# Kernel optimization log

Measured on AMD Instinct MI355X. Metric: run time of the kernel, lower is better.

The kernel has to match this reference:

```python
import jax, jax.numpy as jnp
import numpy as np
from jax import lax

Z_DIM = 64
ZS_SIZE = [[1, 1]] * 12 + [[2, 1]] + [[2, 2]] * 11 + [[4, 2]] + [[4, 4]] * 11  # 36 embeddings
FILTER = [[16, 16]] * 6 + [[16, 32]] + [[32, 32]] * 5 + [[32, 64]] + [[64, 64]] * 5  # 18 blocks
OFFS = np.cumsum([0] + [h * k for h, k in ZS_SIZE]).tolist()  # 242 z-vectors total


def _hyper(Z, hn_w2, hn_b2, hn_w1, hn_b1):
    # Batched HyperNetwork: Z [n, 64] -> kernels [n, 16, 16, 3, 3]
    n = Z.shape[0]
    h_in = (Z @ hn_w2 + hn_b2).reshape(n, 16, Z_DIM)            # [n, 16, 64]
    h_fin = jnp.einsum('nid,do->nio', h_in, hn_w1) + hn_b1       # [n, 16, 144]
    return h_fin.reshape(n, 16, 16, 3, 3)


def _make_w(z_all, idx, hn_w2, hn_b2, hn_w1, hn_b1):
    # Assemble conv weight [h*16, k*16, 3, 3] from h*k hypernet tiles (cat dim=1 over k, dim=0 over h)
    h, k = ZS_SIZE[idx]
    Z = z_all[OFFS[idx]:OFFS[idx] + h * k]
    K = _hyper(Z, hn_w2, hn_b2, hn_w1, hn_b1)                    # [h*k, 16, 16, 3, 3]
    K = K.reshape(h, k, 16, 16, 3, 3).transpose(0, 2, 1, 3, 4, 5)
    return K.reshape(h * 16, k * 16, 3, 3)


def _conv(x, w, stride, pad):
    return lax.conv_general_dilated(x, w, (stride, stride), [(pad, pad), (pad, pad)],
                                    dimension_numbers=('NCHW', 'OIHW', 'NCHW'))


def _bn(x, i, g, b, m, v):
    # eval-mode BatchNorm2d with running stats; params padded to 64 channels
    C = x.shape[1]
    gg = g[i, :C].reshape(1, C, 1, 1)
    bb = b[i, :C].reshape(1, C, 1, 1)
    mm = m[i, :C].reshape(1, C, 1, 1)
    vv = v[i, :C].reshape(1, C, 1, 1)
    return (x - mm) * (gg * lax.rsqrt(vv + 1e-5)) + bb


def setup_inputs() -> dict:
    key = jax.random.key(0)
    ks = jax.random.split(key, 16)
    B = 1024
    x = jax.random.normal(ks[0], (B, 3, 32, 32), jnp.float32)
    conv1_w = jax.random.normal(ks[1], (16, 3, 3, 3), jnp.float32) / np.float32(np.sqrt(27.0))
    conv1_b = jnp.zeros((16,), jnp.float32)
    n_bn = 37  # bn1 + 2 per block
    bn_gamma = jnp.ones((n_bn, 64), jnp.float32)
    bn_beta = jnp.zeros((n_bn, 64), jnp.float32)
    bn_mean = jnp.zeros((n_bn, 64), jnp.float32)
    bn_var = jnp.ones((n_bn, 64), jnp.float32)
    hn_w2 = jax.random.normal(ks[2], (Z_DIM, 16 * Z_DIM), jnp.float32) * 0.04
    hn_b2 = jax.random.normal(ks[3], (16 * Z_DIM,), jnp.float32) * 0.01
    hn_w1 = jax.random.normal(ks[4], (Z_DIM, 16 * 9), jnp.float32) * 0.04
    hn_b1 = jax.random.normal(ks[5], (16 * 9,), jnp.float32) * 0.01
    z_all = jax.random.normal(ks[6], (OFFS[-1], Z_DIM), jnp.float32)
    res_w6 = jax.random.normal(ks[7], (32, 16, 1, 1), jnp.float32) * 0.25
    res_b6 = jnp.zeros((32,), jnp.float32)
    res_w12 = jax.random.normal(ks[8], (64, 32, 1, 1), jnp.float32) * 0.18
    res_b12 = jnp.zeros((64,), jnp.float32)
    fin_w = jax.random.normal(ks[9], (10, 64), jnp.float32) * 0.1
    fin_b = jnp.zeros((10,), jnp.float32)
    return {"x": x, "conv1_w": conv1_w, "conv1_b": conv1_b,
            "bn_gamma": bn_gamma, "bn_beta": bn_beta, "bn_mean": bn_mean, "bn_var": bn_var,
            "hn_w2": hn_w2, "hn_b2": hn_b2, "hn_w1": hn_w1, "hn_b1": hn_b1,
            "z_all": z_all, "res_w6": res_w6, "res_b6": res_b6,
            "res_w12": res_w12, "res_b12": res_b12, "fin_w": fin_w, "fin_b": fin_b}


def reference(x, conv1_w, conv1_b, bn_gamma, bn_beta, bn_mean, bn_var,
              hn_w2, hn_b2, hn_w1, hn_b1, z_all,
              res_w6, res_b6, res_w12, res_b12, fin_w, fin_b):
    x = _conv(x, conv1_w, 1, 1) + conv1_b.reshape(1, -1, 1, 1)
    x = jax.nn.relu(_bn(x, 0, bn_gamma, bn_beta, bn_mean, bn_var))
    for i in range(18):
        w1 = _make_w(z_all, 2 * i, hn_w2, hn_b2, hn_w1, hn_b1)
        w2 = _make_w(z_all, 2 * i + 1, hn_w2, hn_b2, hn_w1, hn_b1)
        down = (i > 5 and i % 6 == 0)
        if down:
            rw, rb = (res_w6, res_b6) if i == 6 else (res_w12, res_b12)
            res = _conv(x, rw, 2, 0) + rb.reshape(1, -1, 1, 1)
            stride = 2
        else:
            res = x
            stride = 1
        out = jax.nn.relu(_bn(_conv(x, w1, stride, 1), 1 + 2 * i, bn_gamma, bn_beta, bn_mean, bn_var))
        out = _bn(_conv(out, w2, 1, 1), 2 + 2 * i, bn_gamma, bn_beta, bn_mean, bn_var)
        x = jax.nn.relu(out + res)
    x = x.mean(axis=(2, 3))  # AvgPool2d(8) on [B,64,8,8]
    return x @ fin_w.T + fin_b
```

## Files before the change

### kernel.cpp

```cpp
#include <hip/hip_runtime.h>
#include <hip/hip_bf16.h>


typedef __attribute__((ext_vector_type(8))) short bf16x8;
typedef __attribute__((ext_vector_type(4))) float f32x4;
typedef __attribute__((ext_vector_type(16))) float f32x16;
typedef unsigned short ushort_t;

#define OFFS_LIST {0,1,2,3,4,5,6,7,8,9,10,11,12,14,18,22,26,30,34,38,42,46,50,54,58,66,82,98,114,130,146,162,178,194,210,226,242}
#define K_LIST    {1,1,1,1,1,1,1,1,1,1,1,1,1,2,2,2,2,2,2,2,2,2,2,2,2,4,4,4,4,4,4,4,4,4,4,4}
#define H_LIST    {1,1,1,1,1,1,1,1,1,1,1,1,2,2,2,2,2,2,2,2,2,2,2,2,4,4,4,4,4,4,4,4,4,4,4,4}
#define WOFF_LIST {0,2304,4608,6912,9216,11520,13824,16128,18432,20736,23040,25344,27648,32256,41472,50688,59904,69120,78336,87552,96768,105984,115200,124416,133632,152064,188928,225792,262656,299520,336384,373248,410112,446976,483840,520704}
#define CIN_LIST  {16,16,16,16,16,16,16,16,16,16,16,16,16,32,32,32,32,32,32,32,32,32,32,32,32,64,64,64,64,64,64,64,64,64,64,64}
#define COUT_LIST {16,16,16,16,16,16,16,16,16,16,16,16,32,32,32,32,32,32,32,32,32,32,32,32,64,64,64,64,64,64,64,64,64,64,64,64}
#define WFOFF_LIST {0,7680,15360,23040,30720,38400,46080,53760,61440,69120,76800,84480,92160,107520,139776,170496,201216,231936,262656,293376,324096,354816,385536,416256,446976,508416,637440,760320,883200,1006080,1128960,1251840,1374720,1497600,1620480,1743360}

__constant__ int d_offs[37]  = OFFS_LIST;
__constant__ int d_k[36]     = K_LIST;
__constant__ int d_hh[36]    = H_LIST;
__constant__ int d_woff[36]  = WOFF_LIST;
__constant__ int d_cin[36]   = CIN_LIST;
__constant__ int d_cout[36]  = COUT_LIST;
__constant__ int d_wfoff[36] = WFOFF_LIST;

__device__ inline void split3(float x, ushort_t& h, ushort_t& m, ushort_t& l) {
    unsigned xb = __float_as_uint(x);
    unsigned hb = (xb + 0x8000u) >> 16;
    float fh = __uint_as_float(hb << 16);
    float r = x - fh;
    unsigned mb = (__float_as_uint(r) + 0x8000u) >> 16;
    float fm = __uint_as_float(mb << 16);
    float r2 = r - fm;
    unsigned lb = (__float_as_uint(r2) + 0x8000u) >> 16;
    h = (ushort_t)hb; m = (ushort_t)mb; l = (ushort_t)lb;
}
__device__ inline float b2f(ushort_t u) { return __uint_as_float(((unsigned)u) << 16); }

__global__ void prep(const float* __restrict__ g, const float* __restrict__ be,
                     const float* __restrict__ m, const float* __restrict__ v,
                     const float* __restrict__ rb6, const float* __restrict__ rb12,
                     float* __restrict__ sc, float* __restrict__ sh,
                     float* __restrict__ shp13, float* __restrict__ shp25) {
    int i = blockIdx.x * blockDim.x + threadIdx.x;
    if (i < 2368) {
        float s = g[i] * rsqrtf(v[i] + 1e-5f);
        sc[i] = s;
        sh[i] = be[i] - m[i] * s;
    } else if (i < 2368 + 32) {
        int c = i - 2368;
        int idx2 = 14 * 64 + c;
        float s = g[idx2] * rsqrtf(v[idx2] + 1e-5f);
        shp13[c] = be[idx2] - m[idx2] * s + rb6[c];
    } else if (i < 2400 + 64) {
        int c = i - 2400;
        int idx2 = 26 * 64 + c;
        float s = g[idx2] * rsqrtf(v[idx2] + 1e-5f);
        shp25[c] = be[idx2] - m[idx2] * s + rb12[c];
    }
}

__global__ void hyper_kernel(const float* __restrict__ z_all, const float* __restrict__ w2,
                             const float* __restrict__ b2, const float* __restrict__ w1,
                             const float* __restrict__ b1, const float* __restrict__ bnsc,
                             float* __restrict__ Wg) {
    int n = blockIdx.x;
    int tid = threadIdx.x;
    __shared__ float zrow[64];
    __shared__ float hin[1024];
    if (tid < 64) zrow[tid] = z_all[n * 64 + tid];
    __syncthreads();
    for (int mcol = tid; mcol < 1024; mcol += 256) {
        float acc = b2[mcol];
        #pragma unroll 8
        for (int d = 0; d < 64; ++d) acc += zrow[d] * w2[d * 1024 + mcol];
        hin[mcol] = acc;
    }
    __syncthreads();
    int L = 0;
    while (n >= d_offs[L + 1]) ++L;
    int r = n - d_offs[L];
    int kk = d_k[L];
    int a = r / kk, bb = r % kk;
    int Cin = kk * 16;
    int Cout = d_hh[L] * 16;
    const float* scp = bnsc + (L + 1) * 64;
    float* wp = Wg + d_woff[L];
    for (int e = tid; e < 2304; e += 256) {
        int i = e / 144, o = e % 144;
        int j = o / 9, tap = o % 9;
        float acc = b1[o];
        #pragma unroll 8
        for (int d = 0; d < 64; ++d) acc += hin[i * 64 + d] * w1[d * 144 + o];
        int co = a * 16 + i;
        acc *= scp[co];
        wp[(tap * Cin + (bb * 16 + j)) * Cout + co] = acc;
    }
}

__global__ void split_w(const float* __restrict__ Wg, const float* __restrict__ rw6,
                        const float* __restrict__ rw12, ushort_t* __restrict__ Wf) {
    int L = blockIdx.y;
    int CIN = d_cin[L], COUT = d_cout[L];
    int idx = blockIdx.x * 256 + threadIdx.x;
    int j = idx & 7, lane = (idx >> 3) & 63, t = idx >> 9;
    int hi = lane >> 5;
    float wv;
    int base;
    if (L < 13) {
        int K = 9 * CIN, NKS = (K + 31) / 32, NT = COUT / 16;
        if (t >= NKS * NT) return;
        int nt = t % NT, ks = t / NT;
        int k = ks * 32 + (lane >> 4) * 8 + j;
        int co = nt * 16 + (lane & 15);
        wv = (k < K) ? Wg[d_woff[L] + k * COUT + co] : 0.f;
        base = d_wfoff[L] + ((ks * NT + nt) * 3) * 512 + lane * 8 + j;
    } else {
        int CG8 = CIN / 8, NKS = 5 * CG8, NT = COUT / 32;
        int TKS = NKS + ((L == 25) ? 2 : ((L == 13) ? 1 : 0));
        if (t >= TKS * NT) return;
        int nt = t % NT, ks = t / NT;
        int co = nt * 32 + (lane & 31);
        if (ks < NKS) {
            int o = 2 * ks + hi, tap = o % 10, c8 = o / 10;
            int ci = c8 * 8 + j;
            wv = (tap < 9) ? Wg[d_woff[L] + (tap * CIN + ci) * COUT + co] : 0.f;
        } else if (L == 25) {
            int k = (ks - NKS) * 16 + hi * 8 + j;
            wv = rw12[co * 32 + k];
        } else {
            int k = hi * 8 + j;
            wv = rw6[co * 16 + k];
        }
        base = d_wfoff[L] + ((ks * NT + nt) * 3) * 512 + lane * 8 + j;
    }
    ushort_t h, m, l;
    split3(wv, h, m, l);
    Wf[base] = h; Wf[base + 512] = m; Wf[base + 1024] = l;
}

__global__ void conv_first(const float* __restrict__ x, const float* __restrict__ cw,
                           const float* __restrict__ cb, const float* __restrict__ g,
                           const float* __restrict__ be, const float* __restrict__ m,
                           const float* __restrict__ v, float* __restrict__ out) {
    int idx = blockIdx.x * 256 + threadIdx.x;
    int px = idx & 31; int t = idx >> 5;
    int py = t & 31;   int b = t >> 5;
    float acc[16];
    #pragma unroll
    for (int co = 0; co < 16; ++co) acc[co] = 0.f;
    const float* ip = x + (long)b * 3 * 1024;
    #pragma unroll 1
    for (int ci = 0; ci < 3; ++ci) {
        #pragma unroll 1
        for (int ky = 0; ky < 3; ++ky) {
            int iy = py + ky - 1;
            if ((unsigned)iy >= 32u) continue;
            #pragma unroll
            for (int kx = 0; kx < 3; ++kx) {
                int ix = px + kx - 1;
                if ((unsigned)ix < 32u) {
                    float xv = ip[ci * 1024 + iy * 32 + ix];
                    #pragma unroll
                    for (int co = 0; co < 16; ++co)
                        acc[co] += xv * cw[co * 27 + ci * 9 + ky * 3 + kx];
                }
            }
        }
    }
    long o = ((long)(b * 32 + py) * 32 + px) * 16;
    #pragma unroll
    for (int co = 0; co < 16; ++co) {
        float s = g[co] * rsqrtf(v[co] + 1e-5f);
        float val = (acc[co] + cb[co] - m[co]) * s + be[co];
        out[o + co] = fmaxf(val, 0.f);
    }
}

__global__ void pad_zero_f32(float* __restrict__ buf, int H2, int C4) {
    int idx = blockIdx.x * 256 + threadIdx.x;
    int nb = 2 * H2 + 2 * (H2 - 2);
    int total = 1024 * nb * C4;
    if (idx >= total) return;
    int ch = idx % C4; int t = idx / C4;
    int bp = t % nb; int img = t / nb;
    int y, x;
    if (bp < H2) { y = 0; x = bp; }
    else if (bp < 2 * H2) { y = H2 - 1; x = bp - H2; }
    else { int s = bp - 2 * H2; y = 1 + (s >> 1); x = (s & 1) ? H2 - 1 : 0; }
    long off = (((long)img * H2 + y) * H2 + x) * (C4 * 4) + ch * 4;
    *(float4*)(buf + off) = make_float4(0.f, 0.f, 0.f, 0.f);
}

template<int MODE>
__global__ __launch_bounds__(256) void conv_s1(
        const float* __restrict__ in, const ushort_t* __restrict__ wf,
        const float* __restrict__ shp, const float* __restrict__ res,
        float* __restrict__ out) {
    constexpr int W2 = 34, SLABPIX = 10 * W2;
    constexpr int NKS = 5;

    __shared__ uint4 lds[6 * SLABPIX];

    int tid = threadIdx.x, lane = tid & 63, wid = tid >> 6;
    int g = lane >> 4, r16 = lane & 15;
    int bid = blockIdx.x;
    int img = bid >> 2, blocky = bid & 3;
    int row0 = blocky * 8;

    const ushort_t* wfl = wf + lane * 8;
    bf16x8 wv[NKS][3];
    #pragma unroll
    for (int ks = 0; ks < NKS; ++ks)
        #pragma unroll
        for (int p = 0; p < 3; ++p)
            wv[ks][p] = *(const bf16x8*)(wfl + (ks * 3 + p) * 512);
    #pragma unroll
    for (int ks = 0; ks < NKS; ++ks)
        #pragma unroll
        for (int p = 0; p < 3; ++p)
            asm volatile("" : "+v"(wv[ks][p]));

    const float* ib = in + (long)img * (32 * 32 * 16);
    for (int it = tid; it < SLABPIX * 2; it += 256) {
        int pix = it % SLABPIX, cc = it / SLABPIX;
        int sr = pix / W2, sc = pix % W2;
        int gy = row0 - 1 + sr, gx = sc - 1;
        float vv[8];
        if ((unsigned)gy < 32u && (unsigned)gx < 32u) {
            const float4* p4 = (const float4*)(ib + ((long)gy * 32 + gx) * 16 + cc * 8);
            float4 a0 = p4[0], a1 = p4[1];
            vv[0]=a0.x; vv[1]=a0.y; vv[2]=a0.z; vv[3]=a0.w;
            vv[4]=a1.x; vv[5]=a1.y; vv[6]=a1.z; vv[7]=a1.w;
        } else {
            #pragma unroll
            for (int q = 0; q < 8; ++q) vv[q] = 0.f;
        }
        union { ushort_t u[8]; uint4 q; } H, M, L;
        #pragma unroll
        for (int q = 0; q < 8; ++q) split3(vv[q], H.u[q], M.u[q], L.u[q]);
        lds[(cc * 3 + 0) * SLABPIX + pix] = H.q;
        lds[(cc * 3 + 1) * SLABPIX + pix] = M.q;
        lds[(cc * 3 + 2) * SLABPIX + pix] = L.q;
    }
    __syncthreads();

    int pbase[4];
    #pragma unroll
    for (int mt = 0; mt < 4; ++mt) {
        int pid = (wid * 4 + mt) * 16 + r16;
        pbase[mt] = (pid >> 5) * W2 + (pid & 31);
    }

    f32x4 acc[4] = {};

    #pragma unroll
    for (int ks = 0; ks < NKS; ++ks) {
        int k0 = ks * 32 + g * 8;
        int tap = k0 >> 4;
        int ci8 = (k0 >> 3) & 1;
        int ky = (tap * 11) >> 5;
        int kx = tap - 3 * ky;
        bool dead = (ks == NKS - 1) && (g >= 2);
        int ofs = dead ? 0 : (ci8 * 3) * SLABPIX + ky * W2 + kx;
        #pragma unroll
        for (int mt = 0; mt < 4; ++mt) {
            int e16 = dead ? 0 : ofs + pbase[mt];
            bf16x8 ah = *(const bf16x8*)&lds[e16];
            bf16x8 am = *(const bf16x8*)&lds[e16 + SLABPIX];
            bf16x8 al = *(const bf16x8*)&lds[e16 + 2 * SLABPIX];
            f32x4 c = acc[mt];
            c = __builtin_amdgcn_mfma_f32_16x16x32_bf16(ah, wv[ks][0], c, 0, 0, 0);
            c = __builtin_amdgcn_mfma_f32_16x16x32_bf16(ah, wv[ks][1], c, 0, 0, 0);
            c = __builtin_amdgcn_mfma_f32_16x16x32_bf16(am, wv[ks][0], c, 0, 0, 0);
            c = __builtin_amdgcn_mfma_f32_16x16x32_bf16(ah, wv[ks][2], c, 0, 0, 0);
            c = __builtin_amdgcn_mfma_f32_16x16x32_bf16(am, wv[ks][1], c, 0, 0, 0);
            c = __builtin_amdgcn_mfma_f32_16x16x32_bf16(al, wv[ks][0], c, 0, 0, 0);
            acc[mt] = c;
        }
    }

    #pragma unroll
    for (int mt = 0; mt < 4; ++mt) {
        #pragma unroll
        for (int reg = 0; reg < 4; ++reg) {
            int pid = (wid * 4 + mt) * 16 + g * 4 + reg;
            int gy = row0 + (pid >> 5), gx = pid & 31;
            long oidx = (((long)img * 32 + gy) * 32 + gx) * 16 + r16;
            float val = acc[mt][reg] + shp[r16];
            if (MODE == 1) val += res[oidx];
            out[oidx] = fmaxf(val, 0.f);
        }
    }
}

template<int CIN, int COUT, int HIN, int STRIDE, int TH, int TW, int OUTF>
__global__ __launch_bounds__(256) void conv_mfma(
        const float* __restrict__ in, const ushort_t* __restrict__ wf,
        const float* __restrict__ shp, float* __restrict__ out) {
    constexpr int HOUT = HIN / STRIDE;
    constexpr int H2O = HOUT + 2;
    constexpr int CG8 = CIN / 8;
    constexpr int IH = (TH - 1) * STRIDE + 3;
    constexpr int IW = (TW - 1) * STRIDE + 3;
    constexpr int K = 9 * CIN;
    constexpr int NKS = (K + 31) / 32;
    constexpr bool TAIL = (K % 32) != 0;
    constexpr int NT = COUT / 16;
    constexpr int MTW = TH * TW / 64;
    constexpr int PADC = ((2 - (IH * IW)) % 8 + 8) % 8;
    constexpr int CSTU = IH * IW + PADC;
    constexpr int PST = CG8 * CSTU;
    constexpr int TX = HOUT / TW, TY = HOUT / TH;

    __shared__ uint4 lds[3 * PST];

    int tid = threadIdx.x;
    int bid = blockIdx.x;
    int tile = bid % (TY * TX);
    int b = bid / (TY * TX);
    int ty = tile / TX, tx = tile % TX;
    int Y0 = ty * TH, X0 = tx * TW;
    int gy0 = Y0 * STRIDE - 1, gx0 = X0 * STRIDE - 1;

    for (int e = tid; e < CG8 * IH * IW; e += 256) {
        int c8 = e / (IH * IW); int rr = e % (IH * IW);
        int ly = rr / IW, lx = rr % IW;
        int gy = gy0 + ly, gx = gx0 + lx;
        float vv[8];
        if ((unsigned)gy < (unsigned)HIN && (unsigned)gx < (unsigned)HIN) {
            const float4* p = (const float4*)(in + ((long)(b * HIN + gy) * HIN + gx) * CIN + c8 * 8);
            float4 a0 = p[0], a1 = p[1];
            vv[0]=a0.x; vv[1]=a0.y; vv[2]=a0.z; vv[3]=a0.w;
            vv[4]=a1.x; vv[5]=a1.y; vv[6]=a1.z; vv[7]=a1.w;
        } else {
            #pragma unroll
            for (int q = 0; q < 8; ++q) vv[q] = 0.f;
        }
        union { ushort_t u[8]; uint4 q4; } H, M, L;
        #pragma unroll
        for (int q = 0; q < 8; ++q) split3(vv[q], H.u[q], M.u[q], L.u[q]);
        int a16 = c8 * CSTU + rr;
        lds[a16] = H.q4; lds[PST + a16] = M.q4; lds[2 * PST + a16] = L.q4;
    }
    __syncthreads();

    int lane = tid & 63, wid = tid >> 6;
    int g = lane >> 4, r16 = lane & 15;

    f32x4 acc[MTW][NT] = {};

    int pbase[MTW];
    #pragma unroll
    for (int mt = 0; mt < MTW; ++mt) {
        int pid = (wid + 4 * mt) * 16 + r16;
        int py = pid / TW, px = pid % TW;
        pbase[mt] = (py * STRIDE) * IW + px * STRIDE;
    }

    #pragma unroll
    for (int ks = 0; ks < NKS; ++ks) {
        bf16x8 bfr[NT][3];
        #pragma unroll
        for (int nt = 0; nt < NT; ++nt)
            #pragma unroll
            for (int p = 0; p < 3; ++p)
                bfr[nt][p] = *(const bf16x8*)(wf + ((ks * NT + nt) * 3 + p) * 512 + lane * 8);

        int k0 = ks * 32 + g * 8;
        int tap = k0 / CIN;
        int ci8 = (k0 % CIN) >> 3;
        int ky = (tap * 11) >> 5;
        int kx = tap - 3 * ky;
        int ofs = ci8 * CSTU + ky * IW + kx;

        #pragma unroll
        for (int mt = 0; mt < MTW; ++mt) {
            int e16 = ofs + pbase[mt];
            if (TAIL && ks == NKS - 1) e16 = (g < 2) ? e16 : 0;
            const uint4* ap = lds + e16;
            bf16x8 ah = *(const bf16x8*)(ap);
            bf16x8 am = *(const bf16x8*)(ap + PST);
            bf16x8 al = *(const bf16x8*)(ap + 2 * PST);
            #pragma unroll
            for (int nt = 0; nt < NT; ++nt) {
                f32x4 c = acc[mt][nt];
                c = __builtin_amdgcn_mfma_f32_16x16x32_bf16(ah, bfr[nt][0], c, 0, 0, 0);
                c = __builtin_amdgcn_mfma_f32_16x16x32_bf16(ah, bfr[nt][1], c, 0, 0, 0);
                c = __builtin_amdgcn_mfma_f32_16x16x32_bf16(am, bfr[nt][0], c, 0, 0, 0);
                c = __builtin_amdgcn_mfma_f32_16x16x32_bf16(ah, bfr[nt][2], c, 0, 0, 0);
                c = __builtin_amdgcn_mfma_f32_16x16x32_bf16(am, bfr[nt][1], c, 0, 0, 0);
                c = __builtin_amdgcn_mfma_f32_16x16x32_bf16(al, bfr[nt][0], c, 0, 0, 0);
                acc[mt][nt] = c;
            }
        }
    }

    #pragma unroll
    for (int mt = 0; mt < MTW; ++mt) {
        #pragma unroll
        for (int nt = 0; nt < NT; ++nt) {
            int co = nt * 16 + r16;
            float shv = shp[co];
            #pragma unroll
            for (int reg = 0; reg < 4; ++reg) {
                int pid = (wid + 4 * mt) * 16 + g * 4 + reg;
                int py = pid / TW, px = pid % TW;
                int gy = Y0 + py, gx = X0 + px;
                float val = fmaxf(acc[mt][nt][reg] + shv, 0.f);
                if (OUTF == 0) {
                    out[((long)(b * HOUT + gy) * HOUT + gx) * COUT + co] = val;
                } else {
                    out[(((long)b * H2O + gy + 1) * H2O + gx + 1) * COUT + co] = val;
                }
            }
        }
    }
}

template<int CIN, int COUT, int HIN, int STRIDE, int PXB, int MODE, int RKS, int CHUNK>
__global__ __launch_bounds__(256) void conv_s23(
        const float* __restrict__ in, const ushort_t* __restrict__ wf,
        const float* __restrict__ shp, const float* __restrict__ res,
        float* __restrict__ out) {
    constexpr int HOUT = HIN / STRIDE;
    constexpr int H2I = HIN + 2, H2O = HOUT + 2;
    constexpr int C8 = CIN / 8;
    constexpr int NKS = 5 * C8;
    constexpr int TKS = NKS + RKS;
    constexpr int NC = TKS / CHUNK;
    constexpr int NTT = COUT / 32;
    constexpr int ROWSB = PXB / HOUT;
    constexpr int SLABR = (ROWSB - 1) * STRIDE + 3;
    constexpr int SLABPIX = SLABR * H2I;
    constexpr int NBLK = HOUT / ROWSB;
    constexpr int RESU = 3 * C8 * SLABPIX;
    constexpr int LDSU = RESU + ((MODE == 2 || MODE == 3) ? 768 : 0);

    __shared__ uint4 lds[LDSU];

    int tid = threadIdx.x, lane = tid & 63, wid = tid >> 6;
    int lp = lane & 31, hi = lane >> 5;
    int bid = blockIdx.x;
    int img = bid / NBLK, blocky = bid % NBLK;
    int pxg = wid / NTT, ntb = wid % NTT;
    int pix0 = pxg * 32 + lp;
    int py_blk = pix0 / HOUT, px = pix0 % HOUT;
    int py = blocky * ROWSB + py_blk;
    int slabrow0 = blocky * ROWSB * STRIDE;

    const ushort_t* wfl = wf + lane * 8;

    bf16x8 wA[CHUNK][3], wB[CHUNK][3];
    auto LW = [&](int c, bf16x8 (&w)[CHUNK][3]) {
        #pragma unroll
        for (int i = 0; i < CHUNK; ++i) {
            int ks = c * CHUNK + i;
            #pragma unroll
            for (int pp = 0; pp < 3; ++pp)
                w[i][pp] = *(const bf16x8*)(wfl + ((ks * NTT + ntb) * 3 + pp) * 512);
        }
    };

    LW(0, wA);
    if (NC > 1) LW(1, wB);

    const float* ib = in + (long)img * H2I * H2I * CIN;
    for (int it = tid; it < SLABPIX * C8; it += 256) {
        int pix = it % SLABPIX, cc = it / SLABPIX;
        int sr = pix / H2I, sc = pix % H2I;
        const float* p4 = ib + ((long)(slabrow0 + sr) * H2I + sc) * CIN + cc * 8;
        float4 a0 = ((const float4*)p4)[0], a1 = ((const float4*)p4)[1];
        float vv[8] = {a0.x, a0.y, a0.z, a0.w, a1.x, a1.y, a1.z, a1.w};
        union { ushort_t u[8]; uint4 q; } H, M, L;
        #pragma unroll
        for (int q = 0; q < 8; ++q) split3(vv[q], H.u[q], M.u[q], L.u[q]);
        int u0 = cc * 3;
        lds[u0 * SLABPIX + pix] = H.q;
        lds[(u0 + 1) * SLABPIX + pix] = M.q;
        lds[(u0 + 2) * SLABPIX + pix] = L.q;
    }
    if (MODE == 2) {
        for (int it = tid; it < 256; it += 256) {
            int pix = it & 63, cc = it >> 6;
            int ry = pix >> 3, rx = pix & 7;
            const float* r4 = res + (((long)img * 18 + (2 * ry + 1)) * 18 + (2 * rx + 1)) * 32 + cc * 8;
            float4 a0 = ((const float4*)r4)[0], a1 = ((const float4*)r4)[1];
            float vv[8] = {a0.x, a0.y, a0.z, a0.w, a1.x, a1.y, a1.z, a1.w};
            union { ushort_t u[8]; uint4 q; } H, M, L;
            #pragma unroll
            for (int q = 0; q < 8; ++q) split3(vv[q], H.u[q], M.u[q], L.u[q]);
            int u0 = RESU + cc * 3 * 64;
            lds[u0 + pix] = H.q;
            lds[u0 + 64 + pix] = M.q;
            lds[u0 + 128 + pix] = L.q;
        }
    }
    if (MODE == 3) {
        for (int it = tid; it < 256; it += 256) {
            int opix = it >> 1, cg = it & 1;
            int r = opix / 16, cxx = opix % 16;
            int gy = (blocky * 8 + r) * 2, gx = cxx * 2;
            const float* r4 = res + (((long)img * 32 + gy) * 32 + gx) * 16 + cg * 8;
            float4 a0 = ((const float4*)r4)[0], a1 = ((const float4*)r4)[1];
            float vv[8] = {a0.x, a0.y, a0.z, a0.w, a1.x, a1.y, a1.z, a1.w};
            union { ushort_t u[8]; uint4 q; } H, M, L;
            #pragma unroll
            for (int q = 0; q < 8; ++q) split3(vv[q], H.u[q], M.u[q], L.u[q]);
            int u0 = RESU + opix * 6;
            lds[u0 + cg] = H.q;
            lds[u0 + 2 + cg] = M.q;
            lds[u0 + 4 + cg] = L.q;
        }
    }
    __syncthreads();

    int pbase = (py_blk * STRIDE) * H2I + px * STRIDE;
    f32x16 acc = {};

    auto DOC = [&](int c, bf16x8 (&w)[CHUNK][3]) {
        #pragma unroll
        for (int i = 0; i < CHUNK; ++i) {
            int ks = c * CHUNK + i;
            bf16x8 x0, x1, x2;
            if (RKS > 0 && ks >= NKS) {
                if (MODE == 2) {
                    int o2 = 2 * (ks - NKS) + hi;
                    int a = RESU + o2 * 3 * 64 + pix0;
                    x0 = *(const bf16x8*)&lds[a];
                    x1 = *(const bf16x8*)&lds[a + 64];
                    x2 = *(const bf16x8*)&lds[a + 128];
                } else {
                    int a = RESU + pix0 * 6 + hi;
                    x0 = *(const bf16x8*)&lds[a];
                    x1 = *(const bf16x8*)&lds[a + 2];
                    x2 = *(const bf16x8*)&lds[a + 4];
                }
            } else {
                int o = 2 * ks + hi;
                int tap = o % 10, c8i = o / 10;
                int ky = (tap * 11) >> 5, kx = tap - 3 * ky;
                int t16 = (tap == 9) ? 0 : (ky * H2I + kx);
                int a = (c8i * 3) * SLABPIX + pbase + t16;
                x0 = *(const bf16x8*)&lds[a];
                x1 = *(const bf16x8*)&lds[a + SLABPIX];
                x2 = *(const bf16x8*)&lds[a + 2 * SLABPIX];
            }
            acc = __builtin_amdgcn_mfma_f32_32x32x16_bf16(w[i][0], x0, acc, 0, 0, 0);
            acc = __builtin_amdgcn_mfma_f32_32x32x16_bf16(w[i][1], x0, acc, 0, 0, 0);
            acc = __builtin_amdgcn_mfma_f32_32x32x16_bf16(w[i][0], x1, acc, 0, 0, 0);
            acc = __builtin_amdgcn_mfma_f32_32x32x16_bf16(w[i][2], x0, acc, 0, 0, 0);
            acc = __builtin_amdgcn_mfma_f32_32x32x16_bf16(w[i][1], x1, acc, 0, 0, 0);
            acc = __builtin_amdgcn_mfma_f32_32x32x16_bf16(w[i][0], x2, acc, 0, 0, 0);
        }
    };

    #pragma unroll 1
    for (int c = 0; c < NC; c += 2) {
        DOC(c, wA);
        if (c + 2 < NC) LW(c + 2, wA);
        if (c + 1 < NC) { DOC(c + 1, wB); if (c + 3 < NC) LW(c + 3, wB); }
    }

    float* ob = out + (((long)img * H2O + py + 1) * H2O + (px + 1)) * COUT;
    #pragma unroll
    for (int g = 0; g < 4; ++g) {
        int co = ntb * 32 + g * 8 + 4 * hi;
        float v0 = acc[4 * g + 0] + shp[co + 0];
        float v1 = acc[4 * g + 1] + shp[co + 1];
        float v2 = acc[4 * g + 2] + shp[co + 2];
        float v3 = acc[4 * g + 3] + shp[co + 3];
        *(float4*)(ob + co) = make_float4(fmaxf(v0, 0.f), fmaxf(v1, 0.f),
                                          fmaxf(v2, 0.f), fmaxf(v3, 0.f));
    }
}

template<int CIN, int HIN, int TPW>
__global__ __launch_bounds__(256) void block_fused(
        const float* __restrict__ in, const ushort_t* __restrict__ wf1,
        const ushort_t* __restrict__ wf2, const float* __restrict__ sh1,
        const float* __restrict__ sh2, float* __restrict__ out) {
    constexpr int H2 = HIN + 2, H2PIX = H2 * H2;
    constexpr int C8 = CIN / 8;
    constexpr int NKS = 5 * C8;
    constexpr int CHUNK = 5, NC = NKS / CHUNK;
    constexpr int NTT = CIN / 32;
    constexpr int BUFU = 3 * C8 * H2PIX;

    __shared__ uint4 lds[BUFU];
    ushort_t* lsh = (ushort_t*)lds;

    int tid = threadIdx.x, lane = tid & 63, wid = tid >> 6;
    int lp = lane & 31, hi = lane >> 5;
    int img = blockIdx.x;

    int ntb0 = (wid * TPW) % NTT;
    int pb[TPW];
    #pragma unroll
    for (int t = 0; t < TPW; ++t) {
        int tl = wid * TPW + t;
        int pix = (tl / NTT) * 32 + lp;
        pb[t] = (pix / HIN + 1) * H2 + (pix % HIN + 1);
    }

    const float* ib = in + (long)img * H2PIX * CIN;
    for (int it = tid; it < H2PIX * C8; it += 256) {
        int cc = it % C8, pix = it / C8;
        const float4* p4 = (const float4*)(ib + (long)pix * CIN + cc * 8);
        float4 a0 = p4[0], a1 = p4[1];
        float vv[8] = {a0.x, a0.y, a0.z, a0.w, a1.x, a1.y, a1.z, a1.w};
        union { ushort_t u[8]; uint4 q; } H, M, L;
        #pragma unroll
        for (int q = 0; q < 8; ++q) split3(vv[q], H.u[q], M.u[q], L.u[q]);
        lds[(cc * 3 + 0) * H2PIX + pix] = H.q;
        lds[(cc * 3 + 1) * H2PIX + pix] = M.q;
        lds[(cc * 3 + 2) * H2PIX + pix] = L.q;
    }
    __syncthreads();

    bf16x8 wA[CHUNK][3], wB[CHUNK][3];
    f32x16 acc[TPW];

    auto CONV = [&](const ushort_t* wf) {
        const ushort_t* wfl = wf + lane * 8;
        #pragma unroll
        for (int t = 0; t < TPW; ++t)
            #pragma unroll
            for (int q = 0; q < 16; ++q) acc[t][q] = 0.f;
        auto LW = [&](int c, bf16x8 (&w)[CHUNK][3]) {
            #pragma unroll
            for (int i = 0; i < CHUNK; ++i) {
                int ks = c * CHUNK + i;
                #pragma unroll
                for (int pp = 0; pp < 3; ++pp)
                    w[i][pp] = *(const bf16x8*)(wfl + ((ks * NTT + ntb0) * 3 + pp) * 512);
            }
        };
        auto DOC = [&](int c, bf16x8 (&w)[CHUNK][3]) {
            #pragma unroll
            for (int i = 0; i < CHUNK; ++i) {
                int ks = c * CHUNK + i;
                int o = 2 * ks + hi;
                int tap = o % 10, c8i = o / 10;
                int ky = (tap * 11) >> 5, kx = tap - 3 * ky;
                int rel = (tap == 9) ? 0 : (ky - 1) * H2 + (kx - 1);
                #pragma unroll
                for (int t = 0; t < TPW; ++t) {
                    int a = (tap == 9) ? (c8i * 3) * H2PIX
                                       : (c8i * 3) * H2PIX + pb[t] + rel;
                    bf16x8 x0 = *(const bf16x8*)&lds[a];
                    bf16x8 x1 = *(const bf16x8*)&lds[a + H2PIX];
                    bf16x8 x2 = *(const bf16x8*)&lds[a + 2 * H2PIX];
                    f32x16 c2 = acc[t];
                    c2 = __builtin_amdgcn_mfma_f32_32x32x16_bf16(w[i][0], x0, c2, 0, 0, 0);
                    c2 = __builtin_amdgcn_mfma_f32_32x32x16_bf16(w[i][1], x0, c2, 0, 0, 0);
                    c2 = __builtin_amdgcn_mfma_f32_32x32x16_bf16(w[i][0], x1, c2, 0, 0, 0);
                    c2 = __builtin_amdgcn_mfma_f32_32x32x16_bf16(w[i][2], x0, c2, 0, 0, 0);
                    c2 = __builtin_amdgcn_mfma_f32_32x32x16_bf16(w[i][1], x1, c2, 0, 0, 0);
                    c2 = __builtin_amdgcn_mfma_f32_32x32x16_bf16(w[i][0], x2, c2, 0, 0, 0);
                    acc[t] = c2;
                }
            }
        };
        LW(0, wA);
        if (NC > 1) LW(1, wB);
        #pragma unroll 1
        for (int c = 0; c < NC; c += 2) {
            DOC(c, wA);
            if (c + 2 < NC) LW(c + 2, wA);
            if (c + 1 < NC) { DOC(c + 1, wB); if (c + 3 < NC) LW(c + 3, wB); }
        }
    };

    CONV(wf1);
    __syncthreads();
    #pragma unroll
    for (int t = 0; t < TPW; ++t) {
        #pragma unroll
        for (int q = 0; q < 4; ++q) {
            int co = ntb0 * 32 + q * 8 + 4 * hi;
            int c8o = co >> 3;
            ushort4 h4, m4, l4;
            #pragma unroll
            for (int e = 0; e < 4; ++e) {
                float val = fmaxf(acc[t][4 * q + e] + sh1[co + e], 0.f);
                ushort_t h, m2, l;
                split3(val, h, m2, l);
                ((ushort_t*)&h4)[e] = h; ((ushort_t*)&m4)[e] = m2; ((ushort_t*)&l4)[e] = l;
            }
            int so = (((c8o * 3) * H2PIX + pb[t]) << 3) + (co & 7);
            *(ushort4*)&lsh[so] = h4;
            *(ushort4*)&lsh[so + H2PIX * 8] = m4;
            *(ushort4*)&lsh[so + 2 * H2PIX * 8] = l4;
        }
    }
    __syncthreads();

    CONV(wf2);
    float* ob = out + (long)img * H2PIX * CIN;
    #pragma unroll
    for (int t = 0; t < TPW; ++t) {
        #pragma unroll
        for (int q = 0; q < 4; ++q) {
            int co = ntb0 * 32 + q * 8 + 4 * hi;
            float4 r = *(const float4*)(ib + (long)pb[t] * CIN + co);
            float v0 = acc[t][4 * q + 0] + sh2[co + 0] + r.x;
            float v1 = acc[t][4 * q + 1] + sh2[co + 1] + r.y;
            float v2 = acc[t][4 * q + 2] + sh2[co + 2] + r.z;
            float v3 = acc[t][4 * q + 3] + sh2[co + 3] + r.w;
            *(float4*)(ob + (long)pb[t] * CIN + co) =
                make_float4(fmaxf(v0, 0.f), fmaxf(v1, 0.f), fmaxf(v2, 0.f), fmaxf(v3, 0.f));
        }
    }
}

__global__ void pool_fc(const float* __restrict__ X, const float* __restrict__ fw,
                        const float* __restrict__ fb, float* __restrict__ out) {
    int b = blockIdx.x;
    int c = threadIdx.x;
    float s = 0.f;
    #pragma unroll
    for (int p = 0; p < 64; ++p) {
        int y = p >> 3, x = p & 7;
        s += X[(((long)b * 10 + y + 1) * 10 + (x + 1)) * 64 + c];
    }
    __shared__ float pooled[64];
    pooled[c] = s * (1.f / 64.f);
    __syncthreads();
    if (c < 10) {
        float acc = fb[c];
        #pragma unroll
        for (int k = 0; k < 64; ++k) acc += pooled[k] * fw[c * 64 + k];
        out[b * 10 + c] = acc;
    }
}

extern "C" void kernel_launch(void* const* d_in, const int* in_sizes, int n_in,
                              void* d_out, int out_size, void* d_ws, size_t ws_size,
                              hipStream_t stream) {
    const float* x       = (const float*)d_in[0];
    const float* conv1_w = (const float*)d_in[1];
    const float* conv1_b = (const float*)d_in[2];
    const float* bn_g    = (const float*)d_in[3];
    const float* bn_b    = (const float*)d_in[4];
    const float* bn_m    = (const float*)d_in[5];
    const float* bn_v    = (const float*)d_in[6];
    const float* hn_w2   = (const float*)d_in[7];
    const float* hn_b2   = (const float*)d_in[8];
    const float* hn_w1   = (const float*)d_in[9];
    const float* hn_b1   = (const float*)d_in[10];
    const float* z_all   = (const float*)d_in[11];
    const float* res_w6  = (const float*)d_in[12];
    const float* res_b6  = (const float*)d_in[13];
    const float* res_w12 = (const float*)d_in[14];
    const float* res_b12 = (const float*)d_in[15];
    const float* fin_w   = (const float*)d_in[16];
    const float* fin_b   = (const float*)d_in[17];
    float* outp = (float*)d_out;

    float* wsf      = (float*)d_ws;
    float* Wg       = wsf;
    float* bnsc     = wsf + 557568;
    float* bnsh     = wsf + 559936;
    float* shp13    = wsf + 562304;
    float* shp25    = wsf + 564864;
    ushort_t* Wfrag = (ushort_t*)(wsf + 565248);

    float* A0f = (float*)((char*)d_ws + (size_t)(16) * (1 << 20));
    float* A1f = (float*)((char*)d_ws + (size_t)(80) * (1 << 20));
    float* A2f = (float*)((char*)d_ws + (size_t)(144) * (1 << 20));

    static const int wfoff[36] = WFOFF_LIST;

    prep<<<20, 256, 0, stream>>>(bn_g, bn_b, bn_m, bn_v, res_b6, res_b12,
                                 bnsc, bnsh, shp13, shp25);
    hyper_kernel<<<242, 256, 0, stream>>>(z_all, hn_w2, hn_b2, hn_w1, hn_b1, bnsc, Wg);
    split_w<<<dim3(168, 36), 256, 0, stream>>>(Wg, res_w6, res_w12, Wfrag);
    conv_first<<<4096, 256, 0, stream>>>(x, conv1_w, conv1_b, bn_g, bn_b, bn_m, bn_v, A0f);

    float* X = A0f; float* T1 = A1f; float* T2 = A2f;
    for (int i = 0; i < 6; ++i) {
        int L1 = 2 * i, L2 = 2 * i + 1;
        conv_s1<0><<<4096, 256, 0, stream>>>(
            X, Wfrag + wfoff[L1], bnsh + (L1 + 1) * 64, nullptr, T1);
        conv_s1<1><<<4096, 256, 0, stream>>>(
            T1, Wfrag + wfoff[L2], bnsh + (L2 + 1) * 64, X, T2);
        float* tmp = X; X = T2; T2 = tmp;
    }
    pad_zero_f32<<<2176, 256, 0, stream>>>(A1f, 18, 8);
    conv_mfma<16,32,32,2,8,16,1><<<2048, 256, 0, stream>>>(
        A0f, Wfrag + wfoff[12], bnsh + 13 * 64, A1f);
    pad_zero_f32<<<2176, 256, 0, stream>>>(A2f, 18, 8);
    conv_s23<32,32,16,1,128,3,1,3><<<2048, 256, 0, stream>>>(
        A1f, Wfrag + wfoff[13], shp13, A0f, A2f);

    X = A2f; T1 = A1f;
    for (int i = 7; i < 12; ++i) {
        int L1 = 2 * i, L2 = 2 * i + 1;
        block_fused<32,16,2><<<1024, 256, 0, stream>>>(
            X, Wfrag + wfoff[L1], Wfrag + wfoff[L2],
            bnsh + (L1 + 1) * 64, bnsh + (L2 + 1) * 64, T1);
        float* tmp = X; X = T1; T1 = tmp;
    }
    pad_zero_f32<<<2304, 256, 0, stream>>>(A0f, 10, 16);
    conv_s23<32,64,16,2,64,0,0,5><<<1024, 256, 0, stream>>>(
        A1f, Wfrag + wfoff[24], bnsh + 25 * 64, nullptr, A0f);
    pad_zero_f32<<<2304, 256, 0, stream>>>(A2f, 10, 16);
    conv_s23<64,64,8,1,64,2,2,6><<<1024, 256, 0, stream>>>(
        A0f, Wfrag + wfoff[25], shp25, A1f, A2f);

    X = A2f; T1 = A0f;
    for (int i = 13; i < 18; ++i) {
        int L1 = 2 * i, L2 = 2 * i + 1;
        block_fused<64,8,1><<<1024, 256, 0, stream>>>(
            X, Wfrag + wfoff[L1], Wfrag + wfoff[L2],
            bnsh + (L1 + 1) * 64, bnsh + (L2 + 1) * 64, T1);
        float* tmp = X; X = T1; T1 = tmp;
    }
    pool_fc<<<1024, 64, 0, stream>>>(A0f, fin_w, fin_b, outp);
}
```

Before: 1.291 ms.

## Fuse both convs of each stage-1 residual block and add split-row stage-2 kernel

Stage-1 residual blocks now run as one kernel per block instead of two. Each workgroup loads a 12-row halo slab, computes the first conv on 10 rows (with recompute), writes the intermediate back into LDS as bf16 triples, then computes the second conv and adds the residual taken from LDS. This removes the global write and read of the intermediate activation and the separate residual reload. Stage-2 blocks switch from block_fused to a new conv_s2f kernel that splits each image into two halves across 2048 workgroups, uses 32x32 MFMA tiles, and double-buffers the weight chunks. The cost is halo recompute and extra LDS and register pressure.

```diff
diff --git a/kernel.cpp b/kernel.cpp
--- a/kernel.cpp
+++ b/kernel.cpp
@@ -191,40 +191,25 @@
     *(float4*)(buf + off) = make_float4(0.f, 0.f, 0.f, 0.f);
 }
 
-template<int MODE>
-__global__ __launch_bounds__(256) void conv_s1(
-        const float* __restrict__ in, const ushort_t* __restrict__ wf,
-        const float* __restrict__ shp, const float* __restrict__ res,
-        float* __restrict__ out) {
-    constexpr int W2 = 34, SLABPIX = 10 * W2;
+__global__ __launch_bounds__(256) void conv_s1f(
+        const float* __restrict__ in, const ushort_t* __restrict__ wf1,
+        const ushort_t* __restrict__ wf2, const float* __restrict__ sh1,
+        const float* __restrict__ sh2, float* __restrict__ out) {
+    constexpr int W2 = 34, SLABPIX = 12 * W2;
     constexpr int NKS = 5;
-
     __shared__ uint4 lds[6 * SLABPIX];
+    ushort_t* lsh = (ushort_t*)lds;
 
     int tid = threadIdx.x, lane = tid & 63, wid = tid >> 6;
     int g = lane >> 4, r16 = lane & 15;
-    int bid = blockIdx.x;
-    int img = bid >> 2, blocky = bid & 3;
-    int row0 = blocky * 8;
-
-    const ushort_t* wfl = wf + lane * 8;
-    bf16x8 wv[NKS][3];
-    #pragma unroll
-    for (int ks = 0; ks < NKS; ++ks)
-        #pragma unroll
-        for (int p = 0; p < 3; ++p)
-            wv[ks][p] = *(const bf16x8*)(wfl + (ks * 3 + p) * 512);
-    #pragma unroll
-    for (int ks = 0; ks < NKS; ++ks)
-        #pragma unroll
-        for (int p = 0; p < 3; ++p)
-            asm volatile("" : "+v"(wv[ks][p]));
+    int img = blockIdx.x >> 2, by = blockIdx.x & 3;
+    int Y0 = by * 8;
 
     const float* ib = in + (long)img * (32 * 32 * 16);
     for (int it = tid; it < SLABPIX * 2; it += 256) {
         int pix = it % SLABPIX, cc = it / SLABPIX;
         int sr = pix / W2, sc = pix % W2;
-        int gy = row0 - 1 + sr, gx = sc - 1;
+        int gy = Y0 - 2 + sr, gx = sc - 1;
         float vv[8];
         if ((unsigned)gy < 32u && (unsigned)gx < 32u) {
             const float4* p4 = (const float4*)(ib + ((long)gy * 32 + gx) * 16 + cc * 8);
@@ -244,15 +229,28 @@
     }
     __syncthreads();
 
-    int pbase[4];
-    #pragma unroll
-    for (int mt = 0; mt < 4; ++mt) {
-        int pid = (wid * 4 + mt) * 16 + r16;
-        pbase[mt] = (pid >> 5) * W2 + (pid & 31);
-    }
-
-    f32x4 acc[4] = {};
-
+    bf16x8 wv[NKS][3];
+    {
+        const ushort_t* wfl = wf1 + lane * 8;
+        #pragma unroll
+        for (int ks = 0; ks < NKS; ++ks)
+            #pragma unroll
+            for (int p = 0; p < 3; ++p)
+                wv[ks][p] = *(const bf16x8*)(wfl + (ks * 3 + p) * 512);
+        #pragma unroll
+        for (int ks = 0; ks < NKS; ++ks)
+            #pragma unroll
+            for (int p = 0; p < 3; ++p)
+                asm volatile("" : "+v"(wv[ks][p]));
+    }
+
+    int pb1[5];
+    #pragma unroll
+    for (int mt = 0; mt < 5; ++mt) {
+        int pid = (wid * 5 + mt) * 16 + r16;
+        pb1[mt] = (pid >> 5) * W2 + (pid & 31);
+    }
+    f32x4 acc1[5] = {};
     #pragma unroll
     for (int ks = 0; ks < NKS; ++ks) {
         int k0 = ks * 32 + g * 8;
@@ -263,33 +261,316 @@
         bool dead = (ks == NKS - 1) && (g >= 2);
         int ofs = dead ? 0 : (ci8 * 3) * SLABPIX + ky * W2 + kx;
         #pragma unroll
-        for (int mt = 0; mt < 4; ++mt) {
-            int e16 = dead ? 0 : ofs + pbase[mt];
+        for (int mt = 0; mt < 5; ++mt) {
+            int e16 = dead ? 0 : ofs + pb1[mt];
             bf16x8 ah = *(const bf16x8*)&lds[e16];
             bf16x8 am = *(const bf16x8*)&lds[e16 + SLABPIX];
             bf16x8 al = *(const bf16x8*)&lds[e16 + 2 * SLABPIX];
-            f32x4 c = acc[mt];
+            f32x4 c = acc1[mt];
             c = __builtin_amdgcn_mfma_f32_16x16x32_bf16(ah, wv[ks][0], c, 0, 0, 0);
             c = __builtin_amdgcn_mfma_f32_16x16x32_bf16(ah, wv[ks][1], c, 0, 0, 0);
             c = __builtin_amdgcn_mfma_f32_16x16x32_bf16(am, wv[ks][0], c, 0, 0, 0);
             c = __builtin_amdgcn_mfma_f32_16x16x32_bf16(ah, wv[ks][2], c, 0, 0, 0);
             c = __builtin_amdgcn_mfma_f32_16x16x32_bf16(am, wv[ks][1], c, 0, 0, 0);
             c = __builtin_amdgcn_mfma_f32_16x16x32_bf16(al, wv[ks][0], c, 0, 0, 0);
-            acc[mt] = c;
-        }
-    }
-
+            acc1[mt] = c;
+        }
+    }
+
+    int ccR = r16 >> 3, elR = r16 & 7;
+    float res[4][4];
     #pragma unroll
     for (int mt = 0; mt < 4; ++mt) {
         #pragma unroll
         for (int reg = 0; reg < 4; ++reg) {
             int pid = (wid * 4 + mt) * 16 + g * 4 + reg;
-            int gy = row0 + (pid >> 5), gx = pid & 31;
+            int spix = ((pid >> 5) + 2) * W2 + (pid & 31) + 1;
+            int b0 = ((ccR * 3) * SLABPIX + spix) * 8 + elR;
+            res[mt][reg] = b2f(lsh[b0]) + b2f(lsh[b0 + SLABPIX * 8])
+                         + b2f(lsh[b0 + 2 * SLABPIX * 8]);
+        }
+    }
+    __syncthreads();
+
+    #pragma unroll
+    for (int mt = 0; mt < 5; ++mt) {
+        #pragma unroll
+        for (int reg = 0; reg < 4; ++reg) {
+            int pid = (wid * 5 + mt) * 16 + g * 4 + reg;
+            int prow = pid >> 5, pcol = pid & 31;
+            int t = Y0 - 1 + prow;
+            if ((unsigned)t < 32u) {
+                float val = fmaxf(acc1[mt][reg] + sh1[r16], 0.f);
+                ushort_t h, m2, l;
+                split3(val, h, m2, l);
+                int spix = (prow + 1) * W2 + pcol + 1;
+                int b0 = ((ccR * 3) * SLABPIX + spix) * 8 + elR;
+                lsh[b0] = h;
+                lsh[b0 + SLABPIX * 8] = m2;
+                lsh[b0 + 2 * SLABPIX * 8] = l;
+            }
+        }
+    }
+    __syncthreads();
+
+    {
+        const ushort_t* wfl = wf2 + lane * 8;
+        #pragma unroll
+        for (int ks = 0; ks < NKS; ++ks)
+            #pragma unroll
+            for (int p = 0; p < 3; ++p)
+                wv[ks][p] = *(const bf16x8*)(wfl + (ks * 3 + p) * 512);
+        #pragma unroll
+        for (int ks = 0; ks < NKS; ++ks)
+            #pragma unroll
+            for (int p = 0; p < 3; ++p)
+                asm volatile("" : "+v"(wv[ks][p]));
+    }
+    int pb2[4];
+    #pragma unroll
+    for (int mt = 0; mt < 4; ++mt) {
+        int pid = (wid * 4 + mt) * 16 + r16;
+        pb2[mt] = ((pid >> 5) + 1) * W2 + (pid & 31);
+    }
+    f32x4 acc2[4] = {};
+    #pragma unroll
+    for (int ks = 0; ks < NKS; ++ks) {
+        int k0 = ks * 32 + g * 8;
+        int tap = k0 >> 4;
+        int ci8 = (k0 >> 3) & 1;
+        int ky = (tap * 11) >> 5;
+        int kx = tap - 3 * ky;
+        bool dead = (ks == NKS - 1) && (g >= 2);
+        int ofs = dead ? 0 : (ci8 * 3) * SLABPIX + ky * W2 + kx;
+        #pragma unroll
+        for (int mt = 0; mt < 4; ++mt) {
+            int e16 = dead ? 0 : ofs + pb2[mt];
+            bf16x8 ah = *(const bf16x8*)&lds[e16];
+            bf16x8 am = *(const bf16x8*)&lds[e16 + SLABPIX];
+            bf16x8 al = *(const bf16x8*)&lds[e16 + 2 * SLABPIX];
+            f32x4 c = acc2[mt];
+            c = __builtin_amdgcn_mfma_f32_16x16x32_bf16(ah, wv[ks][0], c, 0, 0, 0);
+            c = __builtin_amdgcn_mfma_f32_16x16x32_bf16(ah, wv[ks][1], c, 0, 0, 0);
+            c = __builtin_amdgcn_mfma_f32_16x16x32_bf16(am, wv[ks][0], c, 0, 0, 0);
+            c = __builtin_amdgcn_mfma_f32_16x16x32_bf16(ah, wv[ks][2], c, 0, 0, 0);
+            c = __builtin_amdgcn_mfma_f32_16x16x32_bf16(am, wv[ks][1], c, 0, 0, 0);
+            c = __builtin_amdgcn_mfma_f32_16x16x32_bf16(al, wv[ks][0], c, 0, 0, 0);
+            acc2[mt] = c;
+        }
+    }
+
+    #pragma unroll
+    for (int mt = 0; mt < 4; ++mt) {
+        #pragma unroll
+        for (int reg = 0; reg < 4; ++reg) {
+            int pid = (wid * 4 + mt) * 16 + g * 4 + reg;
+            int gy = Y0 + (pid >> 5), gx = pid & 31;
             long oidx = (((long)img * 32 + gy) * 32 + gx) * 16 + r16;
-            float val = acc[mt][reg] + shp[r16];
-            if (MODE == 1) val += res[oidx];
+            float val = acc2[mt][reg] + sh2[r16] + res[mt][reg];
             out[oidx] = fmaxf(val, 0.f);
         }
+    }
+}
+
+__global__ __launch_bounds__(256) void conv_s2f(
+        const float* __restrict__ in, const ushort_t* __restrict__ wf1,
+        const ushort_t* __restrict__ wf2, const float* __restrict__ sh1,
+        const float* __restrict__ sh2, float* __restrict__ out) {
+    constexpr int H2 = 18, SLABPIX = 11 * H2;
+    constexpr int C8 = 4, NKS = 20, CHUNK = 5, NC = 4;
+    __shared__ uint4 lds[12 * SLABPIX];
+    ushort_t* lsh = (ushort_t*)lds;
+
+    int tid = threadIdx.x, lane = tid & 63, wid = tid >> 6;
+    int lp = lane & 31, hi = lane >> 5;
+    int img = blockIdx.x >> 1, half = blockIdx.x & 1;
+    int S = half ? 7 : 0;
+    int Y0 = half * 8;
+    int ODELTA = Y0 + 1 - S;
+
+    const float* ib = in + (long)img * (H2 * H2 * 32);
+    for (int it = tid; it < SLABPIX * C8; it += 256) {
+        int pix = it % SLABPIX, cc = it / SLABPIX;
+        int sr = pix / H2, sc = pix % H2;
+        const float* p4 = ib + ((long)(S + sr) * H2 + sc) * 32 + cc * 8;
+        float4 a0 = ((const float4*)p4)[0], a1 = ((const float4*)p4)[1];
+        float vv[8] = {a0.x, a0.y, a0.z, a0.w, a1.x, a1.y, a1.z, a1.w};
+        union { ushort_t u[8]; uint4 q; } H, M, L;
+        #pragma unroll
+        for (int q = 0; q < 8; ++q) split3(vv[q], H.u[q], M.u[q], L.u[q]);
+        lds[(cc * 3 + 0) * SLABPIX + pix] = H.q;
+        lds[(cc * 3 + 1) * SLABPIX + pix] = M.q;
+        lds[(cc * 3 + 2) * SLABPIX + pix] = L.q;
+    }
+    __syncthreads();
+
+    bf16x8 wA[CHUNK][3], wB[CHUNK][3];
+
+    int pTA = wid * 32 + lp;
+    int trA = pTA >> 4, tcA = pTA & 15;
+    int pbA = trA * H2 + tcA;
+    int pTB = 4 * 32 + lp;
+    int trB = pTB >> 4, tcB = pTB & 15;
+    int pbB = (trB < 9) ? trB * H2 + tcB : 0;
+    bool w0 = (wid == 0);
+
+    f32x16 accA = {}, accB = {};
+    {
+        const ushort_t* wfl = wf1 + lane * 8;
+        auto LW = [&](int c, bf16x8 (&w)[CHUNK][3]) {
+            #pragma unroll
+            for (int i = 0; i < CHUNK; ++i) {
+                int ks = c * CHUNK + i;
+                #pragma unroll
+                for (int pp = 0; pp < 3; ++pp)
+                    w[i][pp] = *(const bf16x8*)(wfl + (ks * 3 + pp) * 512);
+            }
+        };
+        auto DOC = [&](int c, bf16x8 (&w)[CHUNK][3]) {
+            #pragma unroll
+            for (int i = 0; i < CHUNK; ++i) {
+                int ks = c * CHUNK + i;
+                int o = 2 * ks + hi;
+                int tap = o % 10, c8i = o / 10;
+                int ky = (tap * 11) >> 5, kx = tap - 3 * ky;
+                int t16 = (tap == 9) ? 0 : (ky * H2 + kx);
+                int base = (c8i * 3) * SLABPIX + t16;
+                {
+                    int a = base + pbA;
+                    bf16x8 x0 = *(const bf16x8*)&lds[a];
+                    bf16x8 x1 = *(const bf16x8*)&lds[a + SLABPIX];
+                    bf16x8 x2 = *(const bf16x8*)&lds[a + 2 * SLABPIX];
+                    f32x16 c2 = accA;
+                    c2 = __builtin_amdgcn_mfma_f32_32x32x16_bf16(w[i][0], x0, c2, 0, 0, 0);
+                    c2 = __builtin_amdgcn_mfma_f32_32x32x16_bf16(w[i][1], x0, c2, 0, 0, 0);
+                    c2 = __builtin_amdgcn_mfma_f32_32x32x16_bf16(w[i][0], x1, c2, 0, 0, 0);
+                    c2 = __builtin_amdgcn_mfma_f32_32x32x16_bf16(w[i][2], x0, c2, 0, 0, 0);
+                    c2 = __builtin_amdgcn_mfma_f32_32x32x16_bf16(w[i][1], x1, c2, 0, 0, 0);
+                    c2 = __builtin_amdgcn_mfma_f32_32x32x16_bf16(w[i][0], x2, c2, 0, 0, 0);
+                    accA = c2;
+                }
+                if (w0) {
+                    int a = base + pbB;
+                    bf16x8 x0 = *(const bf16x8*)&lds[a];
+                    bf16x8 x1 = *(const bf16x8*)&lds[a + SLABPIX];
+                    bf16x8 x2 = *(const bf16x8*)&lds[a + 2 * SLABPIX];
+                    f32x16 c2 = accB;
+                    c2 = __builtin_amdgcn_mfma_f32_32x32x16_bf16(w[i][0], x0, c2, 0, 0, 0);
+                    c2 = __builtin_amdgcn_mfma_f32_32x32x16_bf16(w[i][1], x0, c2, 0, 0, 0);
+                    c2 = __builtin_amdgcn_mfma_f32_32x32x16_bf16(w[i][0], x1, c2, 0, 0, 0);
+                    c2 = __builtin_amdgcn_mfma_f32_32x32x16_bf16(w[i][2], x0, c2, 0, 0, 0);
+                    c2 = __builtin_amdgcn_mfma_f32_32x32x16_bf16(w[i][1], x1, c2, 0, 0, 0);
+                    c2 = __builtin_amdgcn_mfma_f32_32x32x16_bf16(w[i][0], x2, c2, 0, 0, 0);
+                    accB = c2;
+                }
+            }
+        };
+        LW(0, wA); LW(1, wB);
+        #pragma unroll 1
+        for (int c = 0; c < NC; c += 2) {
+            DOC(c, wA);
+            if (c + 2 < NC) LW(c + 2, wA);
+            DOC(c + 1, wB);
+            if (c + 3 < NC) LW(c + 3, wB);
+        }
+    }
+
+    int orow = (wid * 32 + lp) >> 4, ocol = lp & 15;
+    int spixR = (orow + ODELTA) * H2 + ocol + 1;
+    float res[4][4];
+    #pragma unroll
+    for (int q = 0; q < 4; ++q) {
+        #pragma unroll
+        for (int e = 0; e < 4; ++e) {
+            int co = q * 8 + 4 * hi + e;
+            int b0 = ((q * 3) * SLABPIX + spixR) * 8 + 4 * hi + e;
+            res[q][e] = b2f(lsh[b0]) + b2f(lsh[b0 + SLABPIX * 8])
+                      + b2f(lsh[b0 + 2 * SLABPIX * 8]);
+            (void)co;
+        }
+    }
+    __syncthreads();
+
+    auto WRT = [&](const f32x16& acc, int tr, int tc, bool valid) {
+        if (!valid) return;
+        int spix = (tr + 1) * H2 + tc + 1;
+        #pragma unroll
+        for (int q = 0; q < 4; ++q) {
+            ushort4 h4, m4, l4;
+            #pragma unroll
+            for (int e = 0; e < 4; ++e) {
+                int co = q * 8 + 4 * hi + e;
+                float val = fmaxf(acc[4 * q + e] + sh1[co], 0.f);
+                ushort_t h, m2, l;
+                split3(val, h, m2, l);
+                ((ushort_t*)&h4)[e] = h; ((ushort_t*)&m4)[e] = m2; ((ushort_t*)&l4)[e] = l;
+            }
+            int b0 = ((q * 3) * SLABPIX + spix) * 8 + 4 * hi;
+            *(ushort4*)&lsh[b0] = h4;
+            *(ushort4*)&lsh[b0 + SLABPIX * 8] = m4;
+            *(ushort4*)&lsh[b0 + 2 * SLABPIX * 8] = l4;
+        }
+    };
+    WRT(accA, trA, tcA, true);
+    if (w0) WRT(accB, trB, tcB, trB < 9);
+    __syncthreads();
+
+    int pb2 = (orow + ODELTA - 1) * H2 + ocol;
+    f32x16 acc2 = {};
+    {
+        const ushort_t* wfl = wf2 + lane * 8;
+        auto LW = [&](int c, bf16x8 (&w)[CHUNK][3]) {
+            #pragma unroll
+            for (int i = 0; i < CHUNK; ++i) {
+                int ks = c * CHUNK + i;
+                #pragma unroll
+                for (int pp = 0; pp < 3; ++pp)
+                    w[i][pp] = *(const bf16x8*)(wfl + (ks * 3 + pp) * 512);
+            }
+        };
+        auto DOC = [&](int c, bf16x8 (&w)[CHUNK][3]) {
+            #pragma unroll
+            for (int i = 0; i < CHUNK; ++i) {
+                int ks = c * CHUNK + i;
+                int o = 2 * ks + hi;
+                int tap = o % 10, c8i = o / 10;
+                int ky = (tap * 11) >> 5, kx = tap - 3 * ky;
+                int t16 = (tap == 9) ? 0 : (ky * H2 + kx);
+                int a = (c8i * 3) * SLABPIX + pb2 + t16;
+                bf16x8 x0 = *(const bf16x8*)&lds[a];
+                bf16x8 x1 = *(const bf16x8*)&lds[a + SLABPIX];
+                bf16x8 x2 = *(const bf16x8*)&lds[a + 2 * SLABPIX];
+                f32x16 c2 = acc2;
+                c2 = __builtin_amdgcn_mfma_f32_32x32x16_bf16(w[i][0], x0, c2, 0, 0, 0);
+                c2 = __builtin_amdgcn_mfma_f32_32x32x16_bf16(w[i][1], x0, c2, 0, 0, 0);
+                c2 = __builtin_amdgcn_mfma_f32_32x32x16_bf16(w[i][0], x1, c2, 0, 0, 0);
+                c2 = __builtin_amdgcn_mfma_f32_32x32x16_bf16(w[i][2], x0, c2, 0, 0, 0);
+                c2 = __builtin_amdgcn_mfma_f32_32x32x16_bf16(w[i][1], x1, c2, 0, 0, 0);
+                c2 = __builtin_amdgcn_mfma_f32_32x32x16_bf16(w[i][0], x2, c2, 0, 0, 0);
+                acc2 = c2;
+            }
+        };
+        LW(0, wA); LW(1, wB);
+        #pragma unroll 1
+        for (int c = 0; c < NC; c += 2) {
+            DOC(c, wA);
+            if (c + 2 < NC) LW(c + 2, wA);
+            DOC(c + 1, wB);
+            if (c + 3 < NC) LW(c + 3, wB);
+        }
+    }
+
+    float* ob = out + (long)img * (H2 * H2 * 32)
+              + ((long)(Y0 + orow + 1) * H2 + (ocol + 1)) * 32;
+    #pragma unroll
+    for (int q = 0; q < 4; ++q) {
+        int co = q * 8 + 4 * hi;
+        float v0 = acc2[4 * q + 0] + sh2[co + 0] + res[q][0];
+        float v1 = acc2[4 * q + 1] + sh2[co + 1] + res[q][1];
+        float v2 = acc2[4 * q + 2] + sh2[co + 2] + res[q][2];
+        float v3 = acc2[4 * q + 3] + sh2[co + 3] + res[q][3];
+        *(float4*)(ob + co) = make_float4(fmaxf(v0, 0.f), fmaxf(v1, 0.f),
+                                          fmaxf(v2, 0.f), fmaxf(v3, 0.f));
     }
 }
 
@@ -777,14 +1058,13 @@
     split_w<<<dim3(168, 36), 256, 0, stream>>>(Wg, res_w6, res_w12, Wfrag);
     conv_first<<<4096, 256, 0, stream>>>(x, conv1_w, conv1_b, bn_g, bn_b, bn_m, bn_v, A0f);
 
-    float* X = A0f; float* T1 = A1f; float* T2 = A2f;
+    float* X = A0f; float* T = A1f;
     for (int i = 0; i < 6; ++i) {
         int L1 = 2 * i, L2 = 2 * i + 1;
-        conv_s1<0><<<4096, 256, 0, stream>>>(
-            X, Wfrag + wfoff[L1], bnsh + (L1 + 1) * 64, nullptr, T1);
-        conv_s1<1><<<4096, 256, 0, stream>>>(
-            T1, Wfrag + wfoff[L2], bnsh + (L2 + 1) * 64, X, T2);
-        float* tmp = X; X = T2; T2 = tmp;
+        conv_s1f<<<4096, 256, 0, stream>>>(
+            X, Wfrag + wfoff[L1], Wfrag + wfoff[L2],
+            bnsh + (L1 + 1) * 64, bnsh + (L2 + 1) * 64, T);
+        float* tmp = X; X = T; T = tmp;
     }
     pad_zero_f32<<<2176, 256, 0, stream>>>(A1f, 18, 8);
     conv_mfma<16,32,32,2,8,16,1><<<2048, 256, 0, stream>>>(
@@ -793,13 +1073,13 @@
     conv_s23<32,32,16,1,128,3,1,3><<<2048, 256, 0, stream>>>(
         A1f, Wfrag + wfoff[13], shp13, A0f, A2f);
 
-    X = A2f; T1 = A1f;
+    X = A2f; T = A1f;
     for (int i = 7; i < 12; ++i) {
         int L1 = 2 * i, L2 = 2 * i + 1;
-        block_fused<32,16,2><<<1024, 256, 0, stream>>>(
+        conv_s2f<<<2048, 256, 0, stream>>>(
             X, Wfrag + wfoff[L1], Wfrag + wfoff[L2],
-            bnsh + (L1 + 1) * 64, bnsh + (L2 + 1) * 64, T1);
-        float* tmp = X; X = T1; T1 = tmp;
+            bnsh + (L1 + 1) * 64, bnsh + (L2 + 1) * 64, T);
+        float* tmp = X; X = T; T = tmp;
     }
     pad_zero_f32<<<2304, 256, 0, stream>>>(A0f, 10, 16);
     conv_s23<32,64,16,2,64,0,0,5><<<1024, 256, 0, stream>>>(
@@ -808,13 +1088,13 @@
     conv_s23<64,64,8,1,64,2,2,6><<<1024, 256, 0, stream>>>(
         A0f, Wfrag + wfoff[25], shp25, A1f, A2f);
 
-    X = A2f; T1 = A0f;
+    X = A2f; T = A0f;
     for (int i = 13; i < 18; ++i) {
         int L1 = 2 * i, L2 = 2 * i + 1;
         block_fused<64,8,1><<<1024, 256, 0, stream>>>(
             X, Wfrag + wfoff[L1], Wfrag + wfoff[L2],
-            bnsh + (L1 + 1) * 64, bnsh + (L2 + 1) * 64, T1);
-        float* tmp = X; X = T1; T1 = tmp;
+            bnsh + (L1 + 1) * 64, bnsh + (L2 + 1) * 64, T);
+        float* tmp = X; X = T; T = tmp;
     }
     pool_fc<<<1024, 64, 0, stream>>>(A0f, fin_w, fin_b, outp);
 }
```

Result: slower. 1.404 ms (+8.7%).
